# Optimization experiments

Hardware: AMD Instinct MI355X
Metric: run time of the kernel (lower is better)

Reference implementation:

```python
import jax, jax.numpy as jnp
import numpy as np

EMBED_DIM = 1024
NUM_HEADS = 16
HEAD_DIM = EMBED_DIM // NUM_HEADS


def setup_inputs() -> dict:
    key = jax.random.key(0)
    k1, k2, k3, k4, k5 = jax.random.split(key, 5)
    B, S, D = 4, 2048, EMBED_DIM
    scale = 1.0 / np.sqrt(D)
    qkv = jax.random.normal(k1, (B, S, D), dtype=jnp.float32)
    W_in = jax.random.uniform(k2, (D, 3 * D), dtype=jnp.float32, minval=-scale, maxval=scale)
    b_in = jax.random.uniform(k3, (3 * D,), dtype=jnp.float32, minval=-scale, maxval=scale)
    W_out = jax.random.uniform(k4, (D, D), dtype=jnp.float32, minval=-scale, maxval=scale)
    b_out = jax.random.uniform(k5, (D,), dtype=jnp.float32, minval=-scale, maxval=scale)
    return {"qkv": qkv, "W_in": W_in, "b_in": b_in, "W_out": W_out, "b_out": b_out}


def reference(qkv, W_in, b_in, W_out, b_out):
    B, S, D = qkv.shape
    H, hd = NUM_HEADS, HEAD_DIM
    proj = qkv @ W_in + b_in                      # [B, S, 3D]
    q, k, v = jnp.split(proj, 3, axis=-1)         # each [B, S, D]
    # reshape to heads: [B, H, S, hd]
    q = q.reshape(B, S, H, hd).transpose(0, 2, 1, 3)
    k = k.reshape(B, S, H, hd).transpose(0, 2, 1, 3)
    v = v.reshape(B, S, H, hd).transpose(0, 2, 1, 3)
    scores = jnp.einsum('bhqd,bhkd->bhqk', q, k) / jnp.sqrt(jnp.float32(hd))
    attn = jax.nn.softmax(scores, axis=-1)        # dropout=0.0 -> identity
    ctx = jnp.einsum('bhqk,bhkd->bhqd', attn, v)  # [B, H, S, hd]
    ctx = ctx.transpose(0, 2, 1, 3).reshape(B, S, D)
    return ctx @ W_out + b_out
```

## Files before the change

### kernel.cpp

```cpp
#include <hip/hip_runtime.h>


typedef __bf16 bf16;
typedef __bf16 bf16x4 __attribute__((ext_vector_type(4)));
typedef __bf16 bf16x8 __attribute__((ext_vector_type(8)));
typedef float f32x4 __attribute__((ext_vector_type(4)));

typedef const __attribute__((address_space(1))) void* gas1p;
typedef __attribute__((address_space(3))) void* las3p;
#define GLD16(g, l) __builtin_amdgcn_global_load_lds((gas1p)(g), (las3p)(l), 16, 0, 0)

#if __has_builtin(__builtin_amdgcn_exp2f)
#define EXP2(x) __builtin_amdgcn_exp2f(x)
#else
#define EXP2(x) exp2f(x)
#endif

#define WAITV(n) asm volatile("s_waitcnt vmcnt(" #n ")" ::: "memory")

__device__ __forceinline__ void barp() {
  __builtin_amdgcn_sched_barrier(0);
  __builtin_amdgcn_s_barrier();
  __builtin_amdgcn_sched_barrier(0);
}

__device__ __forceinline__ f32x4 mfma16(bf16x8 a, bf16x8 b, f32x4 c) {
  return __builtin_amdgcn_mfma_f32_16x16x32_bf16(a, b, c, 0, 0, 0);
}

__global__ void prep_kernel(const float* __restrict__ qkv, bf16* __restrict__ Xb,
                            const float* __restrict__ W_in, bf16* __restrict__ WtIn,
                            const float* __restrict__ W_out, bf16* __restrict__ WtOut) {
  __shared__ float tile[32][33];
  int blk = blockIdx.x, tid = threadIdx.x;
  if (blk < 8192) {
    int i = (blk * 256 + tid) * 4;
    float4 v = *(const float4*)(qkv + i);
    bf16x4 o;
    o[0] = (bf16)v.x; o[1] = (bf16)v.y; o[2] = (bf16)v.z; o[3] = (bf16)v.w;
    *(bf16x4*)(Xb + i) = o;
    return;
  }
  const float* in; bf16* out; int R, C, c0, r0;
  if (blk < 11264) {
    int t = blk - 8192; in = W_in; out = WtIn; R = 1024; C = 3072;
    c0 = (t % 96) * 32; r0 = (t / 96) * 32;
  } else {
    int t = blk - 11264; in = W_out; out = WtOut; R = 1024; C = 1024;
    c0 = (t % 32) * 32; r0 = (t / 32) * 32;
  }
  int tx = tid & 31, ty = tid >> 5;
#pragma unroll
  for (int i = 0; i < 4; ++i)
    tile[ty + i * 8][tx] = in[(size_t)(r0 + ty + i * 8) * C + c0 + tx];
  __syncthreads();
#pragma unroll
  for (int i = 0; i < 4; ++i)
    out[(size_t)(c0 + ty + i * 8) * R + r0 + tx] = (bf16)tile[tx][ty + i * 8];
}

__device__ __forceinline__ void stage_mat(const bf16* __restrict__ src, int kt,
                                          char* dst, int tid) {
#pragma unroll
  for (int i = 0; i < 4; ++i) {
    int chunk = i * 256 + tid;
    int row = chunk >> 3;
    int cs = (chunk & 7) ^ (row & 7);
    GLD16(src + (size_t)row * 1024 + kt + cs * 8, dst + chunk * 16);
  }
}

__device__ __forceinline__ void stage_bhalf(const bf16* __restrict__ src, int kt,
                                            char* dst, int tid, int b) {
#pragma unroll
  for (int i = 0; i < 2; ++i) {
    int chunk = (i * 64 + b * 32) * 8 + tid;
    int row = chunk >> 3;
    int cs = (chunk & 7) ^ (row & 7);
    GLD16(src + (size_t)row * 1024 + kt + cs * 8, dst + chunk * 16);
  }
}

__device__ __forceinline__ void gemm_core(
    const bf16* __restrict__ Ab, const bf16* __restrict__ Bb,
    char sA[2][128 * 64 * 2], char sB[2][128 * 64 * 2],
    int tid, int lane, int quad, int wm, int wn, f32x4 (&acc)[4][4]) {
  stage_mat(Ab, 0, sA[0], tid);
  stage_bhalf(Bb, 0, sB[0], tid, 0);
  stage_bhalf(Bb, 0, sB[0], tid, 1);

  for (int t = 0; t < 16; ++t) {
    const int cur = t & 1;
    const int ktn = (t + 1) * 64;
    const char* ca = sA[cur];
    const char* cb = sB[cur];
    char* na = sA[cur ^ 1];
    char* nb = sB[cur ^ 1];

    WAITV(2);
    barp();
    bf16x8 af[4][2], bfr[2][2];
#pragma unroll
    for (int mt = 0; mt < 4; ++mt)
#pragma unroll
      for (int ks = 0; ks < 2; ++ks) {
        int ra = wm + mt * 16 + (lane & 15);
        af[mt][ks] = *(const bf16x8*)(ca + ra * 128 + ((ks * 4 + quad) ^ (ra & 7)) * 16);
      }
#pragma unroll
    for (int j = 0; j < 2; ++j)
#pragma unroll
      for (int ks = 0; ks < 2; ++ks) {
        int rb = wn + j * 16 + (lane & 15);
        bfr[j][ks] = *(const bf16x8*)(cb + rb * 128 + ((ks * 4 + quad) ^ (rb & 7)) * 16);
      }
    if (t < 15) {
      stage_mat(Ab, ktn, na, tid);
      stage_bhalf(Bb, ktn, nb, tid, 0);
    }
    __builtin_amdgcn_s_setprio(1);
#pragma unroll
    for (int ks = 0; ks < 2; ++ks)
#pragma unroll
      for (int mt = 0; mt < 4; ++mt)
#pragma unroll
        for (int j = 0; j < 2; ++j)
          acc[mt][j] = mfma16(af[mt][ks], bfr[j][ks], acc[mt][j]);
    __builtin_amdgcn_s_setprio(0);

    if (t < 15) {
      WAITV(6);
    } else {
      WAITV(0);
    }
    barp();
#pragma unroll
    for (int j = 0; j < 2; ++j)
#pragma unroll
      for (int ks = 0; ks < 2; ++ks) {
        int rb = wn + (2 + j) * 16 + (lane & 15);
        bfr[j][ks] = *(const bf16x8*)(cb + rb * 128 + ((ks * 4 + quad) ^ (rb & 7)) * 16);
      }
    if (t < 15) stage_bhalf(Bb, ktn, nb, tid, 1);
    __builtin_amdgcn_s_setprio(1);
#pragma unroll
    for (int ks = 0; ks < 2; ++ks)
#pragma unroll
      for (int mt = 0; mt < 4; ++mt)
#pragma unroll
        for (int j = 0; j < 2; ++j)
          acc[mt][2 + j] = mfma16(af[mt][ks], bfr[j][ks], acc[mt][2 + j]);
    __builtin_amdgcn_s_setprio(0);
  }
}

__global__ __launch_bounds__(256, 2) void gemm1_kernel(
    const bf16* __restrict__ A, const bf16* __restrict__ Bt, const float* __restrict__ bias,
    bf16* __restrict__ Qo, bf16* __restrict__ Ko, bf16* __restrict__ Vo) {
  __shared__ __align__(16) char sA[2][128 * 64 * 2];
  __shared__ __align__(16) char sB[2][128 * 64 * 2];
  const int tid = threadIdx.x, lane = tid & 63, quad = lane >> 4;
  const int wave = tid >> 6;
  const int id = blockIdx.x, xcd = id & 7, local = id >> 3;
  const int m0 = (xcd * 8 + (local & 7)) * 128, n0 = (local >> 3) * 128;
  const int wm = (wave >> 1) * 64, wn = (wave & 1) * 64;
  f32x4 acc[4][4] = {};

  gemm_core(A + (size_t)m0 * 1024, Bt + (size_t)n0 * 1024, sA, sB,
            tid, lane, quad, wm, wn, acc);

  const int region = n0 >> 10;
#pragma unroll
  for (int nt = 0; nt < 4; ++nt) {
    int n = n0 + wn + nt * 16 + (lane & 15);
    float bv = bias[n];
    int ncol = n & 1023;
    int h = ncol >> 6, d = ncol & 63;
#pragma unroll
    for (int mt = 0; mt < 4; ++mt) {
      int gm = m0 + wm + mt * 16 + quad * 4;
      int bb = gm >> 11, s = gm & 2047;
      if (region == 2) {
        bf16x4 pk;
#pragma unroll
        for (int r = 0; r < 4; ++r) pk[r] = (bf16)(acc[mt][nt][r] + bv);
        *(bf16x4*)(Vo + ((size_t)((bb * 16 + h) * 64 + d)) * 2048 + s) = pk;
      } else {
        bf16* dst = (region == 0) ? Qo : Ko;
        float scl = (region == 0) ? 0.18033688f : 1.0f;
#pragma unroll
        for (int r = 0; r < 4; ++r)
          dst[((size_t)((bb * 16 + h) * 2048) + s + r) * 64 + d] =
              (bf16)((acc[mt][nt][r] + bv) * scl);
      }
    }
  }
}

__global__ __launch_bounds__(256, 2) void flash_kernel(
    const bf16* __restrict__ Q, const bf16* __restrict__ K, const bf16* __restrict__ Vt,
    bf16* __restrict__ ctx) {
  const int n = blockIdx.x;
  const int bh = (n & 7) * 8 + (n >> 6);
  const int qt = (n >> 3) & 7;
  const int b = bh >> 4, h = bh & 15;
  const int tid = threadIdx.x, lane = tid & 63, wave = tid >> 6, quad = lane >> 4;

  __shared__ __align__(16) char sK[2][128 * 64 * 2];
  __shared__ __align__(16) char sV[2][64 * 128 * 2];
  __shared__ __align__(16) char sP[4][64 * 32 * 2];

  const size_t hb = (size_t)bh * 2048 * 64;
  const int q0 = qt * 256;

#pragma unroll
  for (int i = 0; i < 8; ++i) {
    int chunk = i * 256 + tid;
    int row = chunk >> 3;
    int cs = (chunk & 7) ^ (row & 7);
    char* dst = (i < 4) ? (sK[0] + chunk * 16) : (sK[1] + (chunk - 1024) * 16);
    GLD16(Q + hb + (size_t)(q0 + row) * 64 + cs * 8, dst);
  }
  __syncthreads();
  bf16x8 qf[4][2];
#pragma unroll
  for (int j = 0; j < 4; ++j)
#pragma unroll
    for (int ksd = 0; ksd < 2; ++ksd) {
      int row = wave * 64 + j * 16 + (lane & 15);
      const char* src = sK[row >> 7];
      int r128 = row & 127;
      qf[j][ksd] = *(const bf16x8*)(src + r128 * 128 + ((ksd * 4 + quad) ^ (r128 & 7)) * 16);
    }
  __syncthreads();

#pragma unroll
  for (int i = 0; i < 4; ++i) {
    int chunk = i * 256 + tid;
    int row = chunk >> 3;
    int cs = (chunk & 7) ^ (row & 7);
    GLD16(K + hb + (size_t)row * 64 + cs * 8, sK[0] + chunk * 16);
    int vrow = chunk >> 4;
    int vcs = (chunk & 15) ^ (vrow & 7);
    GLD16(Vt + hb + (size_t)vrow * 2048 + vcs * 8, sV[0] + chunk * 16);
  }
  __syncthreads();

  f32x4 ctxa[4][4] = {};
  float l[4] = {0.f, 0.f, 0.f, 0.f};
  char* pw = sP[wave];

  for (int it = 0; it < 16; ++it) {
    const int kv0 = it * 128;
    if (it < 15) {
      char* nk = sK[(it + 1) & 1];
      char* nv = sV[(it + 1) & 1];
#pragma unroll
      for (int i = 0; i < 4; ++i) {
        int chunk = i * 256 + tid;
        int row = chunk >> 3;
        int cs = (chunk & 7) ^ (row & 7);
        GLD16(K + hb + (size_t)(kv0 + 128 + row) * 64 + cs * 8, nk + chunk * 16);
        int vrow = chunk >> 4;
        int vcs = (chunk & 15) ^ (vrow & 7);
        GLD16(Vt + hb + (size_t)vrow * 2048 + kv0 + 128 + vcs * 8, nv + chunk * 16);
      }
    }
    const char* cb = sK[it & 1];
    const char* vb = sV[it & 1];

#pragma unroll
    for (int kq = 0; kq < 4; ++kq) {
      f32x4 st[2][4] = {};
#pragma unroll
      for (int ksd = 0; ksd < 2; ++ksd) {
        bf16x8 kf[2];
#pragma unroll
        for (int ii = 0; ii < 2; ++ii) {
          int row = kq * 32 + ii * 16 + (lane & 15);
          kf[ii] = *(const bf16x8*)(cb + row * 128 + ((ksd * 4 + quad) ^ (row & 7)) * 16);
        }
#pragma unroll
        for (int ii = 0; ii < 2; ++ii)
#pragma unroll
          for (int j = 0; j < 4; ++j)
            st[ii][j] = mfma16(kf[ii], qf[j][ksd], st[ii][j]);
      }
#pragma unroll
      for (int ii = 0; ii < 2; ++ii)
#pragma unroll
        for (int j = 0; j < 4; ++j) {
          f32x4 p;
#pragma unroll
          for (int r = 0; r < 4; ++r) {
            p[r] = EXP2(st[ii][j][r]);
            l[j] += p[r];
          }
          bf16x4 pk;
#pragma unroll
          for (int r = 0; r < 4; ++r) pk[r] = (bf16)p[r];
          int q = j * 16 + (lane & 15);
          int s = (ii * 4 + quad) ^ (q & 6);
          *(bf16x4*)(pw + q * 64 + s * 8) = pk;
        }
      bf16x8 pf[4], vf[4];
#pragma unroll
      for (int mt = 0; mt < 4; ++mt) {
        int q = mt * 16 + (lane & 15);
        pf[mt] = *(const bf16x8*)(pw + q * 64 + ((quad ^ ((q >> 1) & 3)) * 16));
      }
#pragma unroll
      for (int nd = 0; nd < 4; ++nd) {
        int row = nd * 16 + (lane & 15);
        vf[nd] = *(const bf16x8*)(vb + row * 256 + (((kq * 4 + quad) ^ (row & 7)) * 16));
      }
#pragma unroll
      for (int mt = 0; mt < 4; ++mt)
#pragma unroll
        for (int nd = 0; nd < 4; ++nd)
          ctxa[mt][nd] = mfma16(pf[mt], vf[nd], ctxa[mt][nd]);
    }
    __syncthreads();
  }

#pragma unroll
  for (int j = 0; j < 4; ++j) {
    l[j] += __shfl_xor(l[j], 16);
    l[j] += __shfl_xor(l[j], 32);
  }
#pragma unroll
  for (int mt = 0; mt < 4; ++mt)
#pragma unroll
    for (int r = 0; r < 4; ++r) {
      float lsh = __shfl(l[mt], quad * 4 + r);
      float rl = __builtin_amdgcn_rcpf(lsh);
      int srow = q0 + wave * 64 + mt * 16 + quad * 4 + r;
#pragma unroll
      for (int nd = 0; nd < 4; ++nd) {
        int col = h * 64 + nd * 16 + (lane & 15);
        ctx[((size_t)(b * 2048 + srow)) * 1024 + col] = (bf16)(ctxa[mt][nd][r] * rl);
      }
    }
}

__global__ __launch_bounds__(256, 2) void gemm2_kernel(
    const bf16* __restrict__ A, const bf16* __restrict__ Bt, const float* __restrict__ bias,
    float* __restrict__ Out) {
  __shared__ __align__(16) char sA[2][128 * 64 * 2];
  __shared__ __align__(16) char sB[2][128 * 64 * 2];
  const int tid = threadIdx.x, lane = tid & 63, quad = lane >> 4;
  const int wave = tid >> 6;
  const int id = blockIdx.x, xcd = id & 7, local = id >> 3;
  const int m0 = (xcd * 8 + (local & 7)) * 128, n0 = (local >> 3) * 128;
  const int wm = (wave >> 1) * 64, wn = (wave & 1) * 64;
  f32x4 acc[4][4] = {};

  gemm_core(A + (size_t)m0 * 1024, Bt + (size_t)n0 * 1024, sA, sB,
            tid, lane, quad, wm, wn, acc);

#pragma unroll
  for (int nt = 0; nt < 4; ++nt) {
    int n = n0 + wn + nt * 16 + (lane & 15);
    float bv = bias[n];
#pragma unroll
    for (int mt = 0; mt < 4; ++mt) {
      int gm = m0 + wm + mt * 16 + quad * 4;
#pragma unroll
      for (int r = 0; r < 4; ++r)
        Out[(size_t)(gm + r) * 1024 + n] = acc[mt][nt][r] + bv;
    }
  }
}

extern "C" void kernel_launch(void* const* d_in, const int* in_sizes, int n_in,
                              void* d_out, int out_size, void* d_ws, size_t ws_size,
                              hipStream_t stream) {
  const float* qkv   = (const float*)d_in[0];
  const float* W_in  = (const float*)d_in[1];
  const float* b_in  = (const float*)d_in[2];
  const float* W_out = (const float*)d_in[3];
  const float* b_out = (const float*)d_in[4];
  float* out = (float*)d_out;

  bf16* Xb    = (bf16*)d_ws;
  bf16* WtIn  = Xb + 8388608;
  bf16* WtOut = WtIn + 3145728;
  bf16* Qb    = WtOut + 1048576;
  bf16* Kb    = Qb + 8388608;
  bf16* Vtb   = Kb + 8388608;
  bf16* Ctx   = Xb;

  prep_kernel<<<12288, 256, 0, stream>>>(qkv, Xb, W_in, WtIn, W_out, WtOut);
  gemm1_kernel<<<1536, 256, 0, stream>>>(Xb, WtIn, b_in, Qb, Kb, Vtb);
  flash_kernel<<<512, 256, 0, stream>>>(Qb, Kb, Vtb, Ctx);
  gemm2_kernel<<<512, 256, 0, stream>>>(Ctx, WtOut, b_out, out);
}
```

Before: 241.3 us.

## Retile QKV projection GEMM to 256x192 tiles with 8 waves and triple-buffered B

The input projection GEMM moves from 128x128 tiles with 256 threads to 256x192 tiles with 512 threads (8 waves, each computing 128x48). A is double-buffered and B is triple-buffered, prefetched two k-steps ahead, and the grid shrinks from 1536 to 512 blocks, which exactly fills 256 CUs twice over. The larger tile raises arithmetic intensity per byte staged and removes the partial last wave of blocks. The cost is more LDS per block (64KB A plus 72KB B), which likely limits occupancy to one block per CU, and heavier register pressure from 24 accumulators per wave.

```diff
diff --git a/kernel.cpp b/kernel.cpp
--- a/kernel.cpp
+++ b/kernel.cpp
@@ -59,6 +59,26 @@
     out[(size_t)(c0 + ty + i * 8) * R + r0 + tx] = (bf16)tile[tx][ty + i * 8];
 }
 
+__device__ __forceinline__ void stage_a256(const bf16* __restrict__ src, int kt,
+                                           char* dst, int tid) {
+#pragma unroll
+  for (int i = 0; i < 4; ++i) {
+    int chunk = i * 512 + tid;
+    int row = chunk >> 3;
+    int cs = (chunk & 7) ^ (row & 7);
+    GLD16(src + (size_t)row * 1024 + kt + cs * 8, dst + chunk * 16);
+  }
+}
+__device__ __forceinline__ void stage_b192(const bf16* __restrict__ src, int kt,
+                                           char* dst, int tid) {
+#pragma unroll
+  for (int i = 0; i < 3; ++i) {
+    int chunk = i * 512 + tid;
+    int row = chunk >> 3;
+    int cs = (chunk & 7) ^ (row & 7);
+    GLD16(src + (size_t)row * 1024 + kt + cs * 8, dst + chunk * 16);
+  }
+}
 __device__ __forceinline__ void stage_mat(const bf16* __restrict__ src, int kt,
                                           char* dst, int tid) {
 #pragma unroll
@@ -69,7 +89,6 @@
     GLD16(src + (size_t)row * 1024 + kt + cs * 8, dst + chunk * 16);
   }
 }
-
 __device__ __forceinline__ void stage_bhalf(const bf16* __restrict__ src, int kt,
                                             char* dst, int tid, int b) {
 #pragma unroll
@@ -81,117 +100,116 @@
   }
 }
 
-__device__ __forceinline__ void gemm_core(
-    const bf16* __restrict__ Ab, const bf16* __restrict__ Bb,
-    char sA[2][128 * 64 * 2], char sB[2][128 * 64 * 2],
-    int tid, int lane, int quad, int wm, int wn, f32x4 (&acc)[4][4]) {
-  stage_mat(Ab, 0, sA[0], tid);
-  stage_bhalf(Bb, 0, sB[0], tid, 0);
-  stage_bhalf(Bb, 0, sB[0], tid, 1);
-
-  for (int t = 0; t < 16; ++t) {
-    const int cur = t & 1;
-    const int ktn = (t + 1) * 64;
-    const char* ca = sA[cur];
-    const char* cb = sB[cur];
-    char* na = sA[cur ^ 1];
-    char* nb = sB[cur ^ 1];
-
-    WAITV(2);
-    barp();
-    bf16x8 af[4][2], bfr[2][2];
-#pragma unroll
-    for (int mt = 0; mt < 4; ++mt)
-#pragma unroll
-      for (int ks = 0; ks < 2; ++ks) {
-        int ra = wm + mt * 16 + (lane & 15);
-        af[mt][ks] = *(const bf16x8*)(ca + ra * 128 + ((ks * 4 + quad) ^ (ra & 7)) * 16);
-      }
-#pragma unroll
-    for (int j = 0; j < 2; ++j)
-#pragma unroll
-      for (int ks = 0; ks < 2; ++ks) {
-        int rb = wn + j * 16 + (lane & 15);
-        bfr[j][ks] = *(const bf16x8*)(cb + rb * 128 + ((ks * 4 + quad) ^ (rb & 7)) * 16);
-      }
-    if (t < 15) {
-      stage_mat(Ab, ktn, na, tid);
-      stage_bhalf(Bb, ktn, nb, tid, 0);
-    }
-    __builtin_amdgcn_s_setprio(1);
-#pragma unroll
-    for (int ks = 0; ks < 2; ++ks)
-#pragma unroll
-      for (int mt = 0; mt < 4; ++mt)
-#pragma unroll
-        for (int j = 0; j < 2; ++j)
-          acc[mt][j] = mfma16(af[mt][ks], bfr[j][ks], acc[mt][j]);
-    __builtin_amdgcn_s_setprio(0);
-
-    if (t < 15) {
-      WAITV(6);
-    } else {
-      WAITV(0);
-    }
-    barp();
-#pragma unroll
-    for (int j = 0; j < 2; ++j)
-#pragma unroll
-      for (int ks = 0; ks < 2; ++ks) {
-        int rb = wn + (2 + j) * 16 + (lane & 15);
-        bfr[j][ks] = *(const bf16x8*)(cb + rb * 128 + ((ks * 4 + quad) ^ (rb & 7)) * 16);
-      }
-    if (t < 15) stage_bhalf(Bb, ktn, nb, tid, 1);
-    __builtin_amdgcn_s_setprio(1);
-#pragma unroll
-    for (int ks = 0; ks < 2; ++ks)
-#pragma unroll
-      for (int mt = 0; mt < 4; ++mt)
-#pragma unroll
-        for (int j = 0; j < 2; ++j)
-          acc[mt][2 + j] = mfma16(af[mt][ks], bfr[j][ks], acc[mt][2 + j]);
-    __builtin_amdgcn_s_setprio(0);
-  }
-}
-
-__global__ __launch_bounds__(256, 2) void gemm1_kernel(
+__global__ __launch_bounds__(512, 2) void gemm1_kernel(
     const bf16* __restrict__ A, const bf16* __restrict__ Bt, const float* __restrict__ bias,
     bf16* __restrict__ Qo, bf16* __restrict__ Ko, bf16* __restrict__ Vo) {
-  __shared__ __align__(16) char sA[2][128 * 64 * 2];
-  __shared__ __align__(16) char sB[2][128 * 64 * 2];
+  __shared__ __align__(16) char sA[2][256 * 64 * 2];
+  __shared__ __align__(16) char sB[3][192 * 64 * 2];
   const int tid = threadIdx.x, lane = tid & 63, quad = lane >> 4;
   const int wave = tid >> 6;
+  const int wm = (wave >> 2) * 128, wn = (wave & 3) * 48;
   const int id = blockIdx.x, xcd = id & 7, local = id >> 3;
-  const int m0 = (xcd * 8 + (local & 7)) * 128, n0 = (local >> 3) * 128;
-  const int wm = (wave >> 1) * 64, wn = (wave & 1) * 64;
-  f32x4 acc[4][4] = {};
-
-  gemm_core(A + (size_t)m0 * 1024, Bt + (size_t)n0 * 1024, sA, sB,
-            tid, lane, quad, wm, wn, acc);
-
-  const int region = n0 >> 10;
-#pragma unroll
-  for (int nt = 0; nt < 4; ++nt) {
-    int n = n0 + wn + nt * 16 + (lane & 15);
+  const int m0 = (xcd * 4 + (local & 3)) * 256, n0 = (local >> 2) * 192;
+  const bf16* Ab = A + (size_t)m0 * 1024;
+  const bf16* Bb = Bt + (size_t)n0 * 1024;
+  f32x4 acc[8][3] = {};
+
+  stage_b192(Bb, 0, sB[0], tid);
+  stage_a256(Ab, 0, sA[0], tid);
+  stage_b192(Bb, 64, sB[1], tid);
+
+  for (int t = 0; t < 16; ++t) {
+    const char* ca = sA[t & 1];
+    const char* cb = sB[t % 3];
+    if (t < 15) { WAITV(3); } else { WAITV(0); }
+    barp();
+
+    bf16x8 af[4][2], b0r[2][2], b1r[2];
+#pragma unroll
+    for (int mtl = 0; mtl < 4; ++mtl)
+#pragma unroll
+      for (int ks = 0; ks < 2; ++ks) {
+        int ra = wm + mtl * 16 + (lane & 15);
+        af[mtl][ks] = *(const bf16x8*)(ca + ra * 128 + ((ks * 4 + quad) ^ (ra & 7)) * 16);
+      }
+#pragma unroll
+    for (int ntl = 0; ntl < 2; ++ntl)
+#pragma unroll
+      for (int ks = 0; ks < 2; ++ks) {
+        int rb = wn + ntl * 16 + (lane & 15);
+        b0r[ntl][ks] = *(const bf16x8*)(cb + rb * 128 + ((ks * 4 + quad) ^ (rb & 7)) * 16);
+      }
+    if (t < 15) stage_a256(Ab, (t + 1) * 64, sA[(t + 1) & 1], tid);
+    if (t < 14) stage_b192(Bb, (t + 2) * 64, sB[(t + 2) % 3], tid);
+    __builtin_amdgcn_s_setprio(1);
+#pragma unroll
+    for (int ks = 0; ks < 2; ++ks)
+#pragma unroll
+      for (int mtl = 0; mtl < 4; ++mtl)
+#pragma unroll
+        for (int ntl = 0; ntl < 2; ++ntl)
+          acc[mtl][ntl] = mfma16(af[mtl][ks], b0r[ntl][ks], acc[mtl][ntl]);
+    __builtin_amdgcn_s_setprio(0);
+
+#pragma unroll
+    for (int ks = 0; ks < 2; ++ks) {
+      int rb = wn + 32 + (lane & 15);
+      b1r[ks] = *(const bf16x8*)(cb + rb * 128 + ((ks * 4 + quad) ^ (rb & 7)) * 16);
+    }
+    __builtin_amdgcn_s_setprio(1);
+#pragma unroll
+    for (int ks = 0; ks < 2; ++ks)
+#pragma unroll
+      for (int mtl = 0; mtl < 4; ++mtl)
+        acc[mtl][2] = mfma16(af[mtl][ks], b1r[ks], acc[mtl][2]);
+    __builtin_amdgcn_s_setprio(0);
+
+#pragma unroll
+    for (int mtl = 0; mtl < 4; ++mtl)
+#pragma unroll
+      for (int ks = 0; ks < 2; ++ks) {
+        int ra = wm + 64 + mtl * 16 + (lane & 15);
+        af[mtl][ks] = *(const bf16x8*)(ca + ra * 128 + ((ks * 4 + quad) ^ (ra & 7)) * 16);
+      }
+    __builtin_amdgcn_s_setprio(1);
+#pragma unroll
+    for (int ks = 0; ks < 2; ++ks)
+#pragma unroll
+      for (int mtl = 0; mtl < 4; ++mtl)
+#pragma unroll
+        for (int ntl = 0; ntl < 2; ++ntl)
+          acc[4 + mtl][ntl] = mfma16(af[mtl][ks], b0r[ntl][ks], acc[4 + mtl][ntl]);
+#pragma unroll
+    for (int ks = 0; ks < 2; ++ks)
+#pragma unroll
+      for (int mtl = 0; mtl < 4; ++mtl)
+        acc[4 + mtl][2] = mfma16(af[mtl][ks], b1r[ks], acc[4 + mtl][2]);
+    __builtin_amdgcn_s_setprio(0);
+  }
+
+#pragma unroll
+  for (int ntl = 0; ntl < 3; ++ntl) {
+    int n = n0 + wn + ntl * 16 + (lane & 15);
     float bv = bias[n];
+    int region = n >> 10;
     int ncol = n & 1023;
     int h = ncol >> 6, d = ncol & 63;
-#pragma unroll
-    for (int mt = 0; mt < 4; ++mt) {
-      int gm = m0 + wm + mt * 16 + quad * 4;
+    float scl = (region == 0) ? 0.18033688f : 1.0f;
+#pragma unroll
+    for (int mtl = 0; mtl < 8; ++mtl) {
+      int gm = m0 + wm + mtl * 16 + quad * 4;
       int bb = gm >> 11, s = gm & 2047;
       if (region == 2) {
         bf16x4 pk;
 #pragma unroll
-        for (int r = 0; r < 4; ++r) pk[r] = (bf16)(acc[mt][nt][r] + bv);
+        for (int r = 0; r < 4; ++r) pk[r] = (bf16)(acc[mtl][ntl][r] + bv);
         *(bf16x4*)(Vo + ((size_t)((bb * 16 + h) * 64 + d)) * 2048 + s) = pk;
       } else {
         bf16* dst = (region == 0) ? Qo : Ko;
-        float scl = (region == 0) ? 0.18033688f : 1.0f;
 #pragma unroll
         for (int r = 0; r < 4; ++r)
           dst[((size_t)((bb * 16 + h) * 2048) + s + r) * 64 + d] =
-              (bf16)((acc[mt][nt][r] + bv) * scl);
+              (bf16)((acc[mtl][ntl][r] + bv) * scl);
       }
     }
   }
@@ -341,6 +359,79 @@
         ctx[((size_t)(b * 2048 + srow)) * 1024 + col] = (bf16)(ctxa[mt][nd][r] * rl);
       }
     }
+}
+
+__device__ __forceinline__ void gemm2_core(
+    const bf16* __restrict__ Ab, const bf16* __restrict__ Bb,
+    char sA[2][128 * 64 * 2], char sB[2][128 * 64 * 2],
+    int tid, int lane, int quad, int wm, int wn, f32x4 (&acc)[4][4]) {
+  stage_mat(Ab, 0, sA[0], tid);
+  stage_bhalf(Bb, 0, sB[0], tid, 0);
+  stage_bhalf(Bb, 0, sB[0], tid, 1);
+
+  for (int t = 0; t < 16; ++t) {
+    const int cur = t & 1;
+    const int ktn = (t + 1) * 64;
+    const char* ca = sA[cur];
+    const char* cb = sB[cur];
+    char* na = sA[cur ^ 1];
+    char* nb = sB[cur ^ 1];
+
+    WAITV(2);
+    barp();
+    bf16x8 af[4][2], bfr[2][2];
+#pragma unroll
+    for (int mt = 0; mt < 4; ++mt)
+#pragma unroll
+      for (int ks = 0; ks < 2; ++ks) {
+        int ra = wm + mt * 16 + (lane & 15);
+        af[mt][ks] = *(const bf16x8*)(ca + ra * 128 + ((ks * 4 + quad) ^ (ra & 7)) * 16);
+      }
+#pragma unroll
+    for (int j = 0; j < 2; ++j)
+#pragma unroll
+      for (int ks = 0; ks < 2; ++ks) {
+        int rb = wn + j * 16 + (lane & 15);
+        bfr[j][ks] = *(const bf16x8*)(cb + rb * 128 + ((ks * 4 + quad) ^ (rb & 7)) * 16);
+      }
+    if (t < 15) {
+      stage_mat(Ab, ktn, na, tid);
+      stage_bhalf(Bb, ktn, nb, tid, 0);
+    }
+    __builtin_amdgcn_s_setprio(1);
+#pragma unroll
+    for (int ks = 0; ks < 2; ++ks)
+#pragma unroll
+      for (int mt = 0; mt < 4; ++mt)
+#pragma unroll
+        for (int j = 0; j < 2; ++j)
+          acc[mt][j] = mfma16(af[mt][ks], bfr[j][ks], acc[mt][j]);
+    __builtin_amdgcn_s_setprio(0);
+
+    if (t < 15) {
+      WAITV(6);
+    } else {
+      WAITV(0);
+    }
+    barp();
+#pragma unroll
+    for (int j = 0; j < 2; ++j)
+#pragma unroll
+      for (int ks = 0; ks < 2; ++ks) {
+        int rb = wn + (2 + j) * 16 + (lane & 15);
+        bfr[j][ks] = *(const bf16x8*)(cb + rb * 128 + ((ks * 4 + quad) ^ (rb & 7)) * 16);
+      }
+    if (t < 15) stage_bhalf(Bb, ktn, nb, tid, 1);
+    __builtin_amdgcn_s_setprio(1);
+#pragma unroll
+    for (int ks = 0; ks < 2; ++ks)
+#pragma unroll
+      for (int mt = 0; mt < 4; ++mt)
+#pragma unroll
+        for (int j = 0; j < 2; ++j)
+          acc[mt][2 + j] = mfma16(af[mt][ks], bfr[j][ks], acc[mt][2 + j]);
+    __builtin_amdgcn_s_setprio(0);
+  }
 }
 
 __global__ __launch_bounds__(256, 2) void gemm2_kernel(
@@ -355,8 +446,8 @@
   const int wm = (wave >> 1) * 64, wn = (wave & 1) * 64;
   f32x4 acc[4][4] = {};
 
-  gemm_core(A + (size_t)m0 * 1024, Bt + (size_t)n0 * 1024, sA, sB,
-            tid, lane, quad, wm, wn, acc);
+  gemm2_core(A + (size_t)m0 * 1024, Bt + (size_t)n0 * 1024, sA, sB,
+             tid, lane, quad, wm, wn, acc);
 
 #pragma unroll
   for (int nt = 0; nt < 4; ++nt) {
@@ -391,7 +482,7 @@
   bf16* Ctx   = Xb;
 
   prep_kernel<<<12288, 256, 0, stream>>>(qkv, Xb, W_in, WtIn, W_out, WtOut);
-  gemm1_kernel<<<1536, 256, 0, stream>>>(Xb, WtIn, b_in, Qb, Kb, Vtb);
+  gemm1_kernel<<<512, 512, 0, stream>>>(Xb, WtIn, b_in, Qb, Kb, Vtb);
   flash_kernel<<<512, 256, 0, stream>>>(Qb, Kb, Vtb, Ctx);
   gemm2_kernel<<<512, 256, 0, stream>>>(Ctx, WtOut, b_out, out);
 }
```

Result: slower. 247.6 us (+2.6%).

## Simplify gemm1 pipeline and stage Q/K epilogue through LDS for coalesced stores

Applied to the files above, without the earlier changes.

gemm1 stops using the split-B-half pipeline with explicit vmcnt waits and instead uses a simpler double-buffered step: prefetch the full next A/B tiles, compute, then __syncthreads. gemm2 keeps the old core under a new name. The Q/K epilogue now writes results into a swizzled LDS scratch region per wave and reads them back as 16-byte vectors, replacing scattered 2-byte global stores with coalesced ones. The LDS round trip and the simpler pipeline may lose some of the load/compute overlap the old schedule had.

```diff
diff --git a/kernel.cpp b/kernel.cpp
--- a/kernel.cpp
+++ b/kernel.cpp
@@ -59,99 +59,42 @@
     out[(size_t)(c0 + ty + i * 8) * R + r0 + tx] = (bf16)tile[tx][ty + i * 8];
 }
 
-__device__ __forceinline__ void stage_mat(const bf16* __restrict__ src, int kt,
-                                          char* dst, int tid) {
+__device__ __forceinline__ void stage_tile(const bf16* __restrict__ src, size_t rstride,
+                                           int kt, char* dst, int tid) {
 #pragma unroll
   for (int i = 0; i < 4; ++i) {
     int chunk = i * 256 + tid;
     int row = chunk >> 3;
     int cs = (chunk & 7) ^ (row & 7);
-    GLD16(src + (size_t)row * 1024 + kt + cs * 8, dst + chunk * 16);
-  }
-}
-
-__device__ __forceinline__ void stage_bhalf(const bf16* __restrict__ src, int kt,
-                                            char* dst, int tid, int b) {
-#pragma unroll
-  for (int i = 0; i < 2; ++i) {
-    int chunk = (i * 64 + b * 32) * 8 + tid;
-    int row = chunk >> 3;
-    int cs = (chunk & 7) ^ (row & 7);
-    GLD16(src + (size_t)row * 1024 + kt + cs * 8, dst + chunk * 16);
-  }
-}
-
-__device__ __forceinline__ void gemm_core(
-    const bf16* __restrict__ Ab, const bf16* __restrict__ Bb,
-    char sA[2][128 * 64 * 2], char sB[2][128 * 64 * 2],
+    GLD16(src + (size_t)row * rstride + kt + cs * 8, dst + chunk * 16);
+  }
+}
+
+__device__ __forceinline__ void gemm_step(
+    const bf16* __restrict__ A, const bf16* __restrict__ B, int m0, int n0,
+    const char* ca, const char* cb, char* na, char* nb, int ktn, bool pref,
     int tid, int lane, int quad, int wm, int wn, f32x4 (&acc)[4][4]) {
-  stage_mat(Ab, 0, sA[0], tid);
-  stage_bhalf(Bb, 0, sB[0], tid, 0);
-  stage_bhalf(Bb, 0, sB[0], tid, 1);
-
-  for (int t = 0; t < 16; ++t) {
-    const int cur = t & 1;
-    const int ktn = (t + 1) * 64;
-    const char* ca = sA[cur];
-    const char* cb = sB[cur];
-    char* na = sA[cur ^ 1];
-    char* nb = sB[cur ^ 1];
-
-    WAITV(2);
-    barp();
-    bf16x8 af[4][2], bfr[2][2];
+  if (pref) {
+    stage_tile(A + (size_t)m0 * 1024, 1024, ktn, na, tid);
+    stage_tile(B + (size_t)n0 * 1024, 1024, ktn, nb, tid);
+  }
+#pragma unroll
+  for (int ks = 0; ks < 2; ++ks) {
+    bf16x8 af[4], bfr[4];
+#pragma unroll
+    for (int t = 0; t < 4; ++t) {
+      int ra = wm + t * 16 + (lane & 15);
+      af[t] = *(const bf16x8*)(ca + ra * 128 + ((ks * 4 + quad) ^ (ra & 7)) * 16);
+      int rb = wn + t * 16 + (lane & 15);
+      bfr[t] = *(const bf16x8*)(cb + rb * 128 + ((ks * 4 + quad) ^ (rb & 7)) * 16);
+    }
 #pragma unroll
     for (int mt = 0; mt < 4; ++mt)
 #pragma unroll
-      for (int ks = 0; ks < 2; ++ks) {
-        int ra = wm + mt * 16 + (lane & 15);
-        af[mt][ks] = *(const bf16x8*)(ca + ra * 128 + ((ks * 4 + quad) ^ (ra & 7)) * 16);
-      }
-#pragma unroll
-    for (int j = 0; j < 2; ++j)
-#pragma unroll
-      for (int ks = 0; ks < 2; ++ks) {
-        int rb = wn + j * 16 + (lane & 15);
-        bfr[j][ks] = *(const bf16x8*)(cb + rb * 128 + ((ks * 4 + quad) ^ (rb & 7)) * 16);
-      }
-    if (t < 15) {
-      stage_mat(Ab, ktn, na, tid);
-      stage_bhalf(Bb, ktn, nb, tid, 0);
-    }
-    __builtin_amdgcn_s_setprio(1);
-#pragma unroll
-    for (int ks = 0; ks < 2; ++ks)
-#pragma unroll
-      for (int mt = 0; mt < 4; ++mt)
-#pragma unroll
-        for (int j = 0; j < 2; ++j)
-          acc[mt][j] = mfma16(af[mt][ks], bfr[j][ks], acc[mt][j]);
-    __builtin_amdgcn_s_setprio(0);
-
-    if (t < 15) {
-      WAITV(6);
-    } else {
-      WAITV(0);
-    }
-    barp();
-#pragma unroll
-    for (int j = 0; j < 2; ++j)
-#pragma unroll
-      for (int ks = 0; ks < 2; ++ks) {
-        int rb = wn + (2 + j) * 16 + (lane & 15);
-        bfr[j][ks] = *(const bf16x8*)(cb + rb * 128 + ((ks * 4 + quad) ^ (rb & 7)) * 16);
-      }
-    if (t < 15) stage_bhalf(Bb, ktn, nb, tid, 1);
-    __builtin_amdgcn_s_setprio(1);
-#pragma unroll
-    for (int ks = 0; ks < 2; ++ks)
-#pragma unroll
-      for (int mt = 0; mt < 4; ++mt)
-#pragma unroll
-        for (int j = 0; j < 2; ++j)
-          acc[mt][2 + j] = mfma16(af[mt][ks], bfr[j][ks], acc[mt][2 + j]);
-    __builtin_amdgcn_s_setprio(0);
-  }
+      for (int nt = 0; nt < 4; ++nt)
+        acc[mt][nt] = mfma16(af[mt], bfr[nt], acc[mt][nt]);
+  }
+  __syncthreads();
 }
 
 __global__ __launch_bounds__(256, 2) void gemm1_kernel(
@@ -166,33 +109,64 @@
   const int wm = (wave >> 1) * 64, wn = (wave & 1) * 64;
   f32x4 acc[4][4] = {};
 
-  gemm_core(A + (size_t)m0 * 1024, Bt + (size_t)n0 * 1024, sA, sB,
-            tid, lane, quad, wm, wn, acc);
+  stage_tile(A + (size_t)m0 * 1024, 1024, 0, sA[0], tid);
+  stage_tile(Bt + (size_t)n0 * 1024, 1024, 0, sB[0], tid);
+  __syncthreads();
+  for (int it = 0; it < 16; it += 2) {
+    gemm_step(A, Bt, m0, n0, sA[0], sB[0], sA[1], sB[1], (it + 1) * 64, true,
+              tid, lane, quad, wm, wn, acc);
+    gemm_step(A, Bt, m0, n0, sA[1], sB[1], sA[0], sB[0], (it + 2) * 64, it + 2 < 16,
+              tid, lane, quad, wm, wn, acc);
+  }
 
   const int region = n0 >> 10;
-#pragma unroll
-  for (int nt = 0; nt < 4; ++nt) {
-    int n = n0 + wn + nt * 16 + (lane & 15);
-    float bv = bias[n];
-    int ncol = n & 1023;
-    int h = ncol >> 6, d = ncol & 63;
-#pragma unroll
-    for (int mt = 0; mt < 4; ++mt) {
-      int gm = m0 + wm + mt * 16 + quad * 4;
-      int bb = gm >> 11, s = gm & 2047;
-      if (region == 2) {
+  if (region == 2) {
+#pragma unroll
+    for (int nt = 0; nt < 4; ++nt) {
+      int n = n0 + wn + nt * 16 + (lane & 15);
+      float bv = bias[n];
+      int ncol = n & 1023;
+      int h = ncol >> 6, d = ncol & 63;
+#pragma unroll
+      for (int mt = 0; mt < 4; ++mt) {
+        int gm = m0 + wm + mt * 16 + quad * 4;
+        int bb = gm >> 11, s = gm & 2047;
         bf16x4 pk;
 #pragma unroll
         for (int r = 0; r < 4; ++r) pk[r] = (bf16)(acc[mt][nt][r] + bv);
         *(bf16x4*)(Vo + ((size_t)((bb * 16 + h) * 64 + d)) * 2048 + s) = pk;
-      } else {
-        bf16* dst = (region == 0) ? Qo : Ko;
-        float scl = (region == 0) ? 0.18033688f : 1.0f;
-#pragma unroll
-        for (int r = 0; r < 4; ++r)
-          dst[((size_t)((bb * 16 + h) * 2048) + s + r) * 64 + d] =
-              (bf16)((acc[mt][nt][r] + bv) * scl);
-      }
+      }
+    }
+  } else {
+    bf16* dst = (region == 0) ? Qo : Ko;
+    const float scl = (region == 0) ? 0.18033688f : 1.0f;
+    char* rp = sA[0] + wave * 8192;
+    const int c = lane & 15;
+#pragma unroll
+    for (int nt = 0; nt < 4; ++nt) {
+      int d_loc = nt * 16 + c;
+      float bv = bias[n0 + wn + d_loc];
+#pragma unroll
+      for (int mt = 0; mt < 4; ++mt) {
+#pragma unroll
+        for (int r = 0; r < 4; ++r) {
+          int s_loc = mt * 16 + quad * 4 + r;
+          int byte = s_loc * 128 + ((d_loc * 2) ^ (((s_loc >> 2) & 3) << 5));
+          *(bf16*)(rp + byte) = (bf16)((acc[mt][nt][r] + bv) * scl);
+        }
+      }
+    }
+    const int h = ((n0 + wn) >> 6) & 15;
+    const int gmb = m0 + wm;
+    const int bb = gmb >> 11;
+    const size_t outbase = ((size_t)(bb * 16 + h)) * 2048 + (gmb & 2047);
+#pragma unroll
+    for (int j = 0; j < 8; ++j) {
+      int srow = j * 8 + (lane >> 3);
+      int chunk = lane & 7;
+      int byte = srow * 128 + ((chunk * 16) ^ (((srow >> 2) & 3) << 5));
+      bf16x8 v = *(const bf16x8*)(rp + byte);
+      *(bf16x8*)(dst + (outbase + srow) * 64 + chunk * 8) = v;
     }
   }
 }
@@ -341,6 +315,100 @@
         ctx[((size_t)(b * 2048 + srow)) * 1024 + col] = (bf16)(ctxa[mt][nd][r] * rl);
       }
     }
+}
+
+__device__ __forceinline__ void stage_mat(const bf16* __restrict__ src, int kt,
+                                          char* dst, int tid) {
+#pragma unroll
+  for (int i = 0; i < 4; ++i) {
+    int chunk = i * 256 + tid;
+    int row = chunk >> 3;
+    int cs = (chunk & 7) ^ (row & 7);
+    GLD16(src + (size_t)row * 1024 + kt + cs * 8, dst + chunk * 16);
+  }
+}
+__device__ __forceinline__ void stage_bhalf(const bf16* __restrict__ src, int kt,
+                                            char* dst, int tid, int b) {
+#pragma unroll
+  for (int i = 0; i < 2; ++i) {
+    int chunk = (i * 64 + b * 32) * 8 + tid;
+    int row = chunk >> 3;
+    int cs = (chunk & 7) ^ (row & 7);
+    GLD16(src + (size_t)row * 1024 + kt + cs * 8, dst + chunk * 16);
+  }
+}
+
+__device__ __forceinline__ void gemm2_core(
+    const bf16* __restrict__ Ab, const bf16* __restrict__ Bb,
+    char sA[2][128 * 64 * 2], char sB[2][128 * 64 * 2],
+    int tid, int lane, int quad, int wm, int wn, f32x4 (&acc)[4][4]) {
+  stage_mat(Ab, 0, sA[0], tid);
+  stage_bhalf(Bb, 0, sB[0], tid, 0);
+  stage_bhalf(Bb, 0, sB[0], tid, 1);
+
+  for (int t = 0; t < 16; ++t) {
+    const int cur = t & 1;
+    const int ktn = (t + 1) * 64;
+    const char* ca = sA[cur];
+    const char* cb = sB[cur];
+    char* na = sA[cur ^ 1];
+    char* nb = sB[cur ^ 1];
+
+    WAITV(2);
+    barp();
+    bf16x8 af[4][2], bfr[2][2];
+#pragma unroll
+    for (int mt = 0; mt < 4; ++mt)
+#pragma unroll
+      for (int ks = 0; ks < 2; ++ks) {
+        int ra = wm + mt * 16 + (lane & 15);
+        af[mt][ks] = *(const bf16x8*)(ca + ra * 128 + ((ks * 4 + quad) ^ (ra & 7)) * 16);
+      }
+#pragma unroll
+    for (int j = 0; j < 2; ++j)
+#pragma unroll
+      for (int ks = 0; ks < 2; ++ks) {
+        int rb = wn + j * 16 + (lane & 15);
+        bfr[j][ks] = *(const bf16x8*)(cb + rb * 128 + ((ks * 4 + quad) ^ (rb & 7)) * 16);
+      }
+    if (t < 15) {
+      stage_mat(Ab, ktn, na, tid);
+      stage_bhalf(Bb, ktn, nb, tid, 0);
+    }
+    __builtin_amdgcn_s_setprio(1);
+#pragma unroll
+    for (int ks = 0; ks < 2; ++ks)
+#pragma unroll
+      for (int mt = 0; mt < 4; ++mt)
+#pragma unroll
+        for (int j = 0; j < 2; ++j)
+          acc[mt][j] = mfma16(af[mt][ks], bfr[j][ks], acc[mt][j]);
+    __builtin_amdgcn_s_setprio(0);
+
+    if (t < 15) {
+      WAITV(6);
+    } else {
+      WAITV(0);
+    }
+    barp();
+#pragma unroll
+    for (int j = 0; j < 2; ++j)
+#pragma unroll
+      for (int ks = 0; ks < 2; ++ks) {
+        int rb = wn + (2 + j) * 16 + (lane & 15);
+        bfr[j][ks] = *(const bf16x8*)(cb + rb * 128 + ((ks * 4 + quad) ^ (rb & 7)) * 16);
+      }
+    if (t < 15) stage_bhalf(Bb, ktn, nb, tid, 1);
+    __builtin_amdgcn_s_setprio(1);
+#pragma unroll
+    for (int ks = 0; ks < 2; ++ks)
+#pragma unroll
+      for (int mt = 0; mt < 4; ++mt)
+#pragma unroll
+        for (int j = 0; j < 2; ++j)
+          acc[mt][2 + j] = mfma16(af[mt][ks], bfr[j][ks], acc[mt][2 + j]);
+    __builtin_amdgcn_s_setprio(0);
+  }
 }
 
 __global__ __launch_bounds__(256, 2) void gemm2_kernel(
@@ -355,8 +423,8 @@
   const int wm = (wave >> 1) * 64, wn = (wave & 1) * 64;
   f32x4 acc[4][4] = {};
 
-  gemm_core(A + (size_t)m0 * 1024, Bt + (size_t)n0 * 1024, sA, sB,
-            tid, lane, quad, wm, wn, acc);
+  gemm2_core(A + (size_t)m0 * 1024, Bt + (size_t)n0 * 1024, sA, sB,
+             tid, lane, quad, wm, wn, acc);
 
 #pragma unroll
   for (int nt = 0; nt < 4; ++nt) {
```

Measured after the change: 250.2 us. 3.7% more time.
